# Performance work log

Hardware: AMD Instinct MI355X
Metric: run time of the kernel (lower is better)

## Reference

```python
import jax, jax.numpy as jnp
import numpy as np

B, T, D = 4, 2048, 1024
H, HS = 16, 64  # n_head, head_size


def setup_inputs() -> dict:
    key = jax.random.key(0)
    ks = jax.random.split(key, 6)
    s_in = 1.0 / np.sqrt(D)
    s_out = 1.0 / np.sqrt(H * HS)
    x = jax.random.normal(ks[0], (B, T, D), dtype=jnp.float32)
    Wq = jax.random.uniform(ks[1], (H, D, HS), jnp.float32, -s_in, s_in)
    Wk = jax.random.uniform(ks[2], (H, D, HS), jnp.float32, -s_in, s_in)
    Wv = jax.random.uniform(ks[3], (H, D, HS), jnp.float32, -s_in, s_in)
    Wo = jax.random.uniform(ks[4], (H * HS, D), jnp.float32, -s_out, s_out)
    bo = jax.random.uniform(ks[5], (D,), jnp.float32, -s_out, s_out)
    return {"x": x, "Wq": Wq, "Wk": Wk, "Wv": Wv, "Wo": Wo, "bo": bo}


def reference(x, Wq, Wk, Wv, Wo, bo):
    # per-head projections, batched across heads: [B,T,D] x [H,D,HS] -> [B,H,T,HS]
    q = jnp.einsum("btd,hde->bhte", x, Wq)
    k = jnp.einsum("btd,hde->bhte", x, Wk)
    v = jnp.einsum("btd,hde->bhte", x, Wv)
    scale = HS ** -0.5
    scores = jnp.einsum("bhqe,bhke->bhqk", q, k) * scale  # [B,H,T,T]
    causal = jnp.tril(jnp.ones((T, T), dtype=bool))
    scores = jnp.where(causal, scores, jnp.float32(-jnp.inf))
    attn = jax.nn.softmax(scores, axis=-1)
    out = jnp.einsum("bhqk,bhke->bhqe", attn, v)  # [B,H,T,HS]
    out = out.transpose(0, 2, 1, 3).reshape(B, T, H * HS)  # concat heads
    return out @ Wo + bo
```

## Files before the change

kernel.cpp:

```cpp
#include <hip/hip_runtime.h>

typedef __attribute__((ext_vector_type(8))) short short8v;
typedef __attribute__((ext_vector_type(4))) short short4v;
typedef __attribute__((ext_vector_type(4))) float floatx4;

namespace {
constexpr int Bn = 4, Tn = 2048, Dn = 1024, Hn = 16, HSn = 64;
}

__device__ __forceinline__ short f2bf(float f) {
  unsigned u = __builtin_bit_cast(unsigned, f);
  u += 0x7fffu + ((u >> 16) & 1u);
  return (short)(u >> 16);
}

__device__ __forceinline__ unsigned pkbf2(float lo, float hi) {
  unsigned r;
  asm("v_cvt_pk_bf16_f32 %0, %1, %2" : "=v"(r) : "v"(lo), "v"(hi));
  return r;
}

typedef const __attribute__((address_space(1))) unsigned int guint_t;
typedef __attribute__((address_space(3))) unsigned int luint_t;

__device__ __forceinline__ void gload16(const void* g, void* l) {
  __builtin_amdgcn_global_load_lds((guint_t*)g, (luint_t*)l, 16, 0, 0);
}

__device__ __forceinline__ short8v rd8(const char* base, int row, int kel) {
  return *(const short8v*)(base + row * 128 + ((kel * 2) ^ ((row & 7) << 4)));
}

__global__ __launch_bounds__(256) void cvt_x_k(const float* __restrict__ x, short* __restrict__ xb) {
  const size_t i = ((size_t)blockIdx.x * 256 + threadIdx.x) * 8;
  const float4 a = *(const float4*)(x + i);
  const float4 b = *(const float4*)(x + i + 4);
  short8v o;
  o[0] = f2bf(a.x); o[1] = f2bf(a.y); o[2] = f2bf(a.z); o[3] = f2bf(a.w);
  o[4] = f2bf(b.x); o[5] = f2bf(b.y); o[6] = f2bf(b.z); o[7] = f2bf(b.w);
  *(short8v*)(xb + i) = o;
}

__global__ __launch_bounds__(256) void tr_wqkv_k(const float* __restrict__ Wq, const float* __restrict__ Wk,
                                                 const float* __restrict__ Wv, short* __restrict__ wt) {
  const int ph = blockIdx.x;
  const int p = ph >> 4, h = ph & 15;
  const int dt = blockIdx.y;
  const float* W = p == 0 ? Wq : p == 1 ? Wk : Wv;
  __shared__ float T[64][65];
  const int t = threadIdx.x;
  const int rr = t >> 2, c0 = (t & 3) * 4;
  const float* src = W + (size_t)h * (Dn * HSn) + (size_t)(dt * 64 + rr) * HSn;
  #pragma unroll
  for (int q = 0; q < 4; ++q) {
    const float4 v = *(const float4*)(src + c0 + q * 16);
    T[rr][c0 + q * 16 + 0] = v.x; T[rr][c0 + q * 16 + 1] = v.y;
    T[rr][c0 + q * 16 + 2] = v.z; T[rr][c0 + q * 16 + 3] = v.w;
  }
  __syncthreads();
  short* dst = wt + ((size_t)p * 1024 + h * 64 + rr) * 1024 + dt * 64;
  #pragma unroll
  for (int q = 0; q < 4; ++q) {
    const int dl = c0 + q * 16;
    short4v ov = {f2bf(T[dl + 0][rr]), f2bf(T[dl + 1][rr]),
                  f2bf(T[dl + 2][rr]), f2bf(T[dl + 3][rr])};
    *(short4v*)(dst + dl) = ov;
  }
}

__global__ __launch_bounds__(256) void tr_wo_k(const float* __restrict__ Wo, short* __restrict__ wot) {
  const int ktile = blockIdx.x, ntile = blockIdx.y;
  __shared__ float T[64][65];
  const int t = threadIdx.x;
  const int rr = t >> 2, c0 = (t & 3) * 4;
  const float* src = Wo + (size_t)(ktile * 64 + rr) * Dn + ntile * 64;
  #pragma unroll
  for (int q = 0; q < 4; ++q) {
    const float4 v = *(const float4*)(src + c0 + q * 16);
    T[rr][c0 + q * 16 + 0] = v.x; T[rr][c0 + q * 16 + 1] = v.y;
    T[rr][c0 + q * 16 + 2] = v.z; T[rr][c0 + q * 16 + 3] = v.w;
  }
  __syncthreads();
  short* dst = wot + (size_t)(ntile * 64 + rr) * 1024 + ktile * 64;
  #pragma unroll
  for (int q = 0; q < 4; ++q) {
    const int dl = c0 + q * 16;
    short4v ov = {f2bf(T[dl + 0][rr]), f2bf(T[dl + 1][rr]),
                  f2bf(T[dl + 2][rr]), f2bf(T[dl + 3][rr])};
    *(short4v*)(dst + dl) = ov;
  }
}

__device__ __forceinline__ void gemm_mainloop(const char* gA, const char* gB, char* As, char* Bs,
                                              floatx4 acc[4][4]) {
  const int tid = threadIdx.x;
  const int wv = tid >> 6, ln = tid & 63;
  const int wr = wv >> 1, wc = wv & 1;
  const int lr = ln >> 3, lg = ln & 7;
  const int fr = ln & 15, kq = ln >> 4;
  for (int kt = 0; kt < 16; ++kt) {
    __syncthreads();
    #pragma unroll
    for (int c = 0; c < 4; ++c) {
      const int r = wv * 32 + c * 8 + lr;
      const int sw = (lg * 16) ^ ((r & 7) * 16);
      gload16(gA + (size_t)r * 2048 + kt * 128 + sw, As + (wv * 32 + c * 8) * 128);
      gload16(gB + (size_t)r * 2048 + kt * 128 + sw, Bs + (wv * 32 + c * 8) * 128);
    }
    __syncthreads();
    #pragma unroll
    for (int kb = 0; kb < 2; ++kb) {
      const int k0 = kb * 32 + kq * 8;
      short8v af[4], bfr[4];
      #pragma unroll
      for (int i = 0; i < 4; ++i) af[i] = rd8(As, wr * 64 + i * 16 + fr, k0);
      #pragma unroll
      for (int j = 0; j < 4; ++j) bfr[j] = rd8(Bs, wc * 64 + j * 16 + fr, k0);
      #pragma unroll
      for (int i = 0; i < 4; ++i)
        #pragma unroll
        for (int j = 0; j < 4; ++j)
          acc[i][j] = __builtin_amdgcn_mfma_f32_16x16x32_bf16(af[i], bfr[j], acc[i][j], 0, 0, 0);
    }
  }
}

__global__ __launch_bounds__(256) void gemm_qkv_k(const short* __restrict__ xb, const short* __restrict__ wt,
                                                  short* __restrict__ qb, short* __restrict__ kb,
                                                  short* __restrict__ vb) {
  __shared__ __align__(16) char As[16384];
  __shared__ __align__(16) char Bs[16384];
  const int m0 = blockIdx.x * 128, n0 = blockIdx.y * 128;
  floatx4 acc[4][4];
  #pragma unroll
  for (int i = 0; i < 4; ++i)
    #pragma unroll
    for (int j = 0; j < 4; ++j) acc[i][j] = floatx4{0.f, 0.f, 0.f, 0.f};
  gemm_mainloop((const char*)xb + (size_t)m0 * 2048, (const char*)wt + (size_t)n0 * 2048, As, Bs, acc);

  const int tid = threadIdx.x, wv = tid >> 6, ln = tid & 63;
  const int wr = wv >> 1, wc = wv & 1;
  const int proj = n0 >> 10;
  const int b = m0 >> 11;
  const int rb_ = (ln >> 4) * 4, fc = ln & 15;
  if (proj < 2) {
    short* dst = proj == 0 ? qb : kb;
    const float sc = proj == 0 ? 0.18033688011112042f : 1.0f;
    #pragma unroll
    for (int i = 0; i < 4; ++i) {
      const int m = m0 + wr * 64 + i * 16 + rb_;
      #pragma unroll
      for (int j = 0; j < 4; ++j) {
        const int n = n0 + wc * 64 + j * 16 + fc;
        const int h = (n >> 6) & 15, e = n & 63;
        short* dp = dst + ((size_t)(b * 16 + h) * Tn + (m & 2047)) * 64 + e;
        #pragma unroll
        for (int r = 0; r < 4; ++r) dp[(size_t)r * 64] = f2bf(acc[i][j][r] * sc);
      }
    }
  } else {
    #pragma unroll
    for (int i = 0; i < 4; ++i) {
      const int m = m0 + wr * 64 + i * 16 + rb_;
      const int t0 = m & 2047;
      #pragma unroll
      for (int j = 0; j < 4; ++j) {
        const int n = n0 + wc * 64 + j * 16 + fc;
        const int h = (n >> 6) & 15, e = n & 63;
        short4v ov = {f2bf(acc[i][j][0]), f2bf(acc[i][j][1]),
                      f2bf(acc[i][j][2]), f2bf(acc[i][j][3])};
        *(short4v*)(vb + ((size_t)(b * 16 + h) * 64 + e) * Tn + t0) = ov;
      }
    }
  }
}

__global__ __launch_bounds__(256) void attn_k(const short* __restrict__ qg, const short* __restrict__ kg,
                                              const short* __restrict__ vg, short* __restrict__ og) {
  __shared__ __align__(16) char Qs[16384];
  __shared__ __align__(16) char Ks[16384];
  __shared__ __align__(16) char Vs[16384];
  char* Ps = Qs;
  const int qt = gridDim.y - 1 - blockIdx.y;
  const int bh = blockIdx.x;
  const int tid = threadIdx.x, wv = tid >> 6, ln = tid & 63;
  const int lr = ln >> 3, lg = ln & 7;
  const int fr = ln & 15, kq = ln >> 4;
  const char* qbase = (const char*)qg + (size_t)bh * Tn * 128;
  const char* kbase = (const char*)kg + (size_t)bh * Tn * 128;
  const char* vbase = (const char*)vg + (size_t)bh * Tn * 128;

  #pragma unroll
  for (int c = 0; c < 4; ++c) {
    const int r = c * 32 + wv * 8 + lr;
    const int sw = (lg * 16) ^ ((r & 7) * 16);
    gload16(qbase + (size_t)(qt * 128 + r) * 128 + sw, Qs + (c * 32 + wv * 8) * 128);
  }
  #pragma unroll
  for (int c = 0; c < 2; ++c) {
    const int r = c * 32 + wv * 8 + lr;
    const int sw = (lg * 16) ^ ((r & 7) * 16);
    gload16(kbase + (size_t)r * 128 + sw, Ks + (c * 32 + wv * 8) * 128);
    gload16(vbase + (size_t)r * 4096 + sw, Vs + (c * 32 + wv * 8) * 128);
  }
  __syncthreads();

  short8v qf[2][2];
  #pragma unroll
  for (int c = 0; c < 2; ++c)
    #pragma unroll
    for (int kb = 0; kb < 2; ++kb)
      qf[c][kb] = rd8(Qs, wv * 32 + c * 16 + fr, kb * 32 + kq * 8);

  short8v ones8;
  #pragma unroll
  for (int i = 0; i < 8; ++i) ones8[i] = (short)0x3F80;

  floatx4 ot[4][2];
  #pragma unroll
  for (int f = 0; f < 4; ++f) { ot[f][0] = floatx4{0.f,0.f,0.f,0.f}; ot[f][1] = floatx4{0.f,0.f,0.f,0.f}; }
  floatx4 lacc[2] = {floatx4{0.f,0.f,0.f,0.f}, floatx4{0.f,0.f,0.f,0.f}};
  float m_i[2] = {-1e30f, -1e30f};

  const int nkt = 2 * qt + 2;
  const int q0w = qt * 128 + wv * 32;
  for (int kt = 0; kt < nkt; ++kt) {
    const int cur = kt & 1;
    if (kt + 1 < nkt) {
      #pragma unroll
      for (int c = 0; c < 2; ++c) {
        const int r = c * 32 + wv * 8 + lr;
        const int sw = (lg * 16) ^ ((r & 7) * 16);
        gload16(kbase + (size_t)((kt + 1) * 64 + r) * 128 + sw,
                Ks + (cur ^ 1) * 8192 + (c * 32 + wv * 8) * 128);
        gload16(vbase + (size_t)r * 4096 + (size_t)(kt + 1) * 128 + sw,
                Vs + (cur ^ 1) * 8192 + (c * 32 + wv * 8) * 128);
      }
    }
    if (kt * 64 <= q0w + 31) {
      const char* Ksc = Ks + cur * 8192;
      const char* Vsc = Vs + cur * 8192;
      floatx4 st[2][4];
      #pragma unroll
      for (int f = 0; f < 4; ++f) { st[0][f] = floatx4{0.f,0.f,0.f,0.f}; st[1][f] = floatx4{0.f,0.f,0.f,0.f}; }
      #pragma unroll
      for (int kb = 0; kb < 2; ++kb) {
        const int e0 = kb * 32 + kq * 8;
        #pragma unroll
        for (int f = 0; f < 4; ++f) {
          const short8v kf = rd8(Ksc, f * 16 + fr, e0);
          st[0][f] = __builtin_amdgcn_mfma_f32_16x16x32_bf16(kf, qf[0][kb], st[0][f], 0, 0, 0);
          st[1][f] = __builtin_amdgcn_mfma_f32_16x16x32_bf16(kf, qf[1][kb], st[1][f], 0, 0, 0);
        }
      }
      if (kt * 64 + 63 > q0w) {
        #pragma unroll
        for (int c = 0; c < 2; ++c) {
          const int q = q0w + c * 16 + fr;
          #pragma unroll
          for (int f = 0; f < 4; ++f)
            #pragma unroll
            for (int r = 0; r < 4; ++r)
              if (kt * 64 + f * 16 + kq * 4 + r > q) st[c][f][r] = -3.0e38f;
        }
      }
      float mx[2];
      #pragma unroll
      for (int c = 0; c < 2; ++c) {
        float v = fmaxf(fmaxf(st[c][0][0], st[c][0][1]), st[c][0][2]);
        v = fmaxf(fmaxf(v, st[c][0][3]), st[c][1][0]);
        v = fmaxf(fmaxf(v, st[c][1][1]), st[c][1][2]);
        v = fmaxf(fmaxf(v, st[c][1][3]), st[c][2][0]);
        v = fmaxf(fmaxf(v, st[c][2][1]), st[c][2][2]);
        v = fmaxf(fmaxf(v, st[c][2][3]), st[c][3][0]);
        v = fmaxf(fmaxf(v, st[c][3][1]), st[c][3][2]);
        v = fmaxf(v, st[c][3][3]);
        v = fmaxf(v, __shfl_xor(v, 16, 64));
        v = fmaxf(v, __shfl_xor(v, 32, 64));
        mx[c] = v;
      }
      const bool noresc = __all((mx[0] <= m_i[0] + 8.f) && (mx[1] <= m_i[1] + 8.f));
      if (!noresc) {
        #pragma unroll
        for (int c = 0; c < 2; ++c) {
          const float mn = fmaxf(m_i[c], mx[c]);
          const float al = exp2f(m_i[c] - mn);
          m_i[c] = mn;
          lacc[c] *= al;
          #pragma unroll
          for (int f = 0; f < 4; ++f) ot[f][c] *= al;
        }
      }
      #pragma unroll
      for (int c = 0; c < 2; ++c) {
        const int prow = wv * 32 + c * 16 + fr;
        #pragma unroll
        for (int f = 0; f < 4; ++f) {
          const float p0 = exp2f(st[c][f][0] - m_i[c]);
          const float p1 = exp2f(st[c][f][1] - m_i[c]);
          const float p2 = exp2f(st[c][f][2] - m_i[c]);
          const float p3 = exp2f(st[c][f][3] - m_i[c]);
          uint2 pv = {pkbf2(p0, p1), pkbf2(p2, p3)};
          *(uint2*)(Ps + prow * 128 + ((f * 32 + kq * 8) ^ ((prow & 7) * 16))) = pv;
        }
      }
      #pragma unroll
      for (int kb = 0; kb < 2; ++kb) {
        const int v0 = kb * 32 + kq * 8;
        const short8v pb0 = rd8(Ps, wv * 32 + fr, v0);
        const short8v pb1 = rd8(Ps, wv * 32 + 16 + fr, v0);
        lacc[0] = __builtin_amdgcn_mfma_f32_16x16x32_bf16(ones8, pb0, lacc[0], 0, 0, 0);
        lacc[1] = __builtin_amdgcn_mfma_f32_16x16x32_bf16(ones8, pb1, lacc[1], 0, 0, 0);
        #pragma unroll
        for (int f = 0; f < 4; ++f) {
          const short8v vf = rd8(Vsc, f * 16 + fr, v0);
          ot[f][0] = __builtin_amdgcn_mfma_f32_16x16x32_bf16(vf, pb0, ot[f][0], 0, 0, 0);
          ot[f][1] = __builtin_amdgcn_mfma_f32_16x16x32_bf16(vf, pb1, ot[f][1], 0, 0, 0);
        }
      }
    }
    __syncthreads();
  }

  const int b = bh >> 4, h = bh & 15;
  #pragma unroll
  for (int c = 0; c < 2; ++c) {
    const float inv = 1.0f / lacc[c][0];
    const size_t t = (size_t)(b * Tn + qt * 128 + wv * 32 + c * 16 + fr);
    #pragma unroll
    for (int f = 0; f < 4; ++f) {
      uint2 o4 = {pkbf2(ot[f][c][0] * inv, ot[f][c][1] * inv),
                  pkbf2(ot[f][c][2] * inv, ot[f][c][3] * inv)};
      *(uint2*)(og + t * 1024 + h * 64 + f * 16 + kq * 4) = o4;
    }
  }
}

__global__ __launch_bounds__(256) void gemm_out_k(const short* __restrict__ ao, const short* __restrict__ wot,
                                                  const float* __restrict__ bo, float* __restrict__ out) {
  __shared__ __align__(16) char As[16384];
  __shared__ __align__(16) char Bs[16384];
  const int m0 = blockIdx.x * 128, n0 = blockIdx.y * 128;
  floatx4 acc[4][4];
  #pragma unroll
  for (int i = 0; i < 4; ++i)
    #pragma unroll
    for (int j = 0; j < 4; ++j) acc[i][j] = floatx4{0.f, 0.f, 0.f, 0.f};
  gemm_mainloop((const char*)ao + (size_t)m0 * 2048, (const char*)wot + (size_t)n0 * 2048, As, Bs, acc);

  const int tid = threadIdx.x, wv = tid >> 6, ln = tid & 63;
  const int wr = wv >> 1, wc = wv & 1;
  const int rb_ = (ln >> 4) * 4, fc = ln & 15;
  #pragma unroll
  for (int i = 0; i < 4; ++i) {
    const int m = m0 + wr * 64 + i * 16 + rb_;
    #pragma unroll
    for (int j = 0; j < 4; ++j) {
      const int n = n0 + wc * 64 + j * 16 + fc;
      const float bias = bo[n];
      #pragma unroll
      for (int r = 0; r < 4; ++r) out[(size_t)(m + r) * Dn + n] = acc[i][j][r] + bias;
    }
  }
}

extern "C" void kernel_launch(void* const* d_in, const int* in_sizes, int n_in,
                              void* d_out, int out_size, void* d_ws, size_t ws_size,
                              hipStream_t stream) {
  const float* x  = (const float*)d_in[0];
  const float* Wq = (const float*)d_in[1];
  const float* Wk = (const float*)d_in[2];
  const float* Wv = (const float*)d_in[3];
  const float* Wo = (const float*)d_in[4];
  const float* bo = (const float*)d_in[5];
  float* out = (float*)d_out;

  char* ws = (char*)d_ws;
  short* xb  = (short*)(ws);
  short* wt  = (short*)(ws + (16u << 20));
  short* wot = (short*)(ws + (22u << 20));
  short* qb  = (short*)(ws + (24u << 20));
  short* kb  = (short*)(ws + (40u << 20));
  short* vb  = (short*)(ws + (56u << 20));
  short* ao  = (short*)(ws + (72u << 20));

  cvt_x_k<<<4096, 256, 0, stream>>>(x, xb);
  tr_wqkv_k<<<dim3(48, 16), 256, 0, stream>>>(Wq, Wk, Wv, wt);
  tr_wo_k<<<dim3(16, 16), 256, 0, stream>>>(Wo, wot);
  gemm_qkv_k<<<dim3(64, 24), 256, 0, stream>>>(xb, wt, qb, kb, vb);
  attn_k<<<dim3(64, 16), 256, 0, stream>>>(qb, kb, vb, ao);
  gemm_out_k<<<dim3(64, 8), 256, 0, stream>>>(ao, wot, bo, out);
}
```

Measured before the change: 190.2 us.

## Keep softmax probabilities in registers and drop Q/P shared-memory staging

The exp'd probability tile is no longer written to and re-read from LDS. The MFMA B operand is built directly from the S accumulator registers, with the key-index order permuted to match the accumulator layout. V fragments are gathered as two 8-byte LDS reads so the permutation holds on that side too. Q is loaded straight from global into registers, removing the Q LDS buffer, and launch bounds request 4 blocks per SM. This saves LDS traffic and a shared round trip, and the smaller LDS footprint raises occupancy, at the cost of narrower V reads and possible register pressure.

```diff
diff --git a/kernel.cpp b/kernel.cpp
--- a/kernel.cpp
+++ b/kernel.cpp
@@ -3,6 +3,8 @@
 typedef __attribute__((ext_vector_type(8))) short short8v;
 typedef __attribute__((ext_vector_type(4))) short short4v;
 typedef __attribute__((ext_vector_type(4))) float floatx4;
+typedef __attribute__((ext_vector_type(4))) unsigned uint4v;
+typedef __attribute__((ext_vector_type(2))) unsigned long long ulong2v;
 
 namespace {
 constexpr int Bn = 4, Tn = 2048, Dn = 1024, Hn = 16, HSn = 64;
@@ -175,12 +177,10 @@
   }
 }
 
-__global__ __launch_bounds__(256) void attn_k(const short* __restrict__ qg, const short* __restrict__ kg,
-                                              const short* __restrict__ vg, short* __restrict__ og) {
-  __shared__ __align__(16) char Qs[16384];
+__global__ __launch_bounds__(256, 4) void attn_k(const short* __restrict__ qg, const short* __restrict__ kg,
+                                                 const short* __restrict__ vg, short* __restrict__ og) {
   __shared__ __align__(16) char Ks[16384];
   __shared__ __align__(16) char Vs[16384];
-  char* Ps = Qs;
   const int qt = gridDim.y - 1 - blockIdx.y;
   const int bh = blockIdx.x;
   const int tid = threadIdx.x, wv = tid >> 6, ln = tid & 63;
@@ -191,26 +191,20 @@
   const char* vbase = (const char*)vg + (size_t)bh * Tn * 128;
 
   #pragma unroll
-  for (int c = 0; c < 4; ++c) {
-    const int r = c * 32 + wv * 8 + lr;
-    const int sw = (lg * 16) ^ ((r & 7) * 16);
-    gload16(qbase + (size_t)(qt * 128 + r) * 128 + sw, Qs + (c * 32 + wv * 8) * 128);
-  }
-  #pragma unroll
   for (int c = 0; c < 2; ++c) {
     const int r = c * 32 + wv * 8 + lr;
     const int sw = (lg * 16) ^ ((r & 7) * 16);
     gload16(kbase + (size_t)r * 128 + sw, Ks + (c * 32 + wv * 8) * 128);
     gload16(vbase + (size_t)r * 4096 + sw, Vs + (c * 32 + wv * 8) * 128);
   }
-  __syncthreads();
-
+
+  const char* qrow0 = qbase + (size_t)(qt * 128 + wv * 32) * 128;
   short8v qf[2][2];
   #pragma unroll
   for (int c = 0; c < 2; ++c)
     #pragma unroll
     for (int kb = 0; kb < 2; ++kb)
-      qf[c][kb] = rd8(Qs, wv * 32 + c * 16 + fr, kb * 32 + kq * 8);
+      qf[c][kb] = *(const short8v*)(qrow0 + (c * 16 + fr) * 128 + kb * 64 + kq * 16);
 
   short8v ones8;
   #pragma unroll
@@ -222,8 +216,11 @@
   floatx4 lacc[2] = {floatx4{0.f,0.f,0.f,0.f}, floatx4{0.f,0.f,0.f,0.f}};
   float m_i[2] = {-1e30f, -1e30f};
 
+  const int swz = (fr & 7) * 16;
   const int nkt = 2 * qt + 2;
   const int q0w = qt * 128 + wv * 32;
+  __syncthreads();
+
   for (int kt = 0; kt < nkt; ++kt) {
     const int cur = kt & 1;
     if (kt + 1 < nkt) {
@@ -291,31 +288,36 @@
           for (int f = 0; f < 4; ++f) ot[f][c] *= al;
         }
       }
-      #pragma unroll
-      for (int c = 0; c < 2; ++c) {
-        const int prow = wv * 32 + c * 16 + fr;
+      short8v pbv[2][2];
+      #pragma unroll
+      for (int c = 0; c < 2; ++c)
+        #pragma unroll
+        for (int kb = 0; kb < 2; ++kb) {
+          uint4v u;
+          u[0] = pkbf2(exp2f(st[c][kb][0] - m_i[c]),     exp2f(st[c][kb][1] - m_i[c]));
+          u[1] = pkbf2(exp2f(st[c][kb][2] - m_i[c]),     exp2f(st[c][kb][3] - m_i[c]));
+          u[2] = pkbf2(exp2f(st[c][kb + 2][0] - m_i[c]), exp2f(st[c][kb + 2][1] - m_i[c]));
+          u[3] = pkbf2(exp2f(st[c][kb + 2][2] - m_i[c]), exp2f(st[c][kb + 2][3] - m_i[c]));
+          pbv[c][kb] = __builtin_bit_cast(short8v, u);
+        }
+      #pragma unroll
+      for (int kb = 0; kb < 2; ++kb) {
+        lacc[0] = __builtin_amdgcn_mfma_f32_16x16x32_bf16(ones8, pbv[0][kb], lacc[0], 0, 0, 0);
+        lacc[1] = __builtin_amdgcn_mfma_f32_16x16x32_bf16(ones8, pbv[1][kb], lacc[1], 0, 0, 0);
+      }
+      #pragma unroll
+      for (int kb = 0; kb < 2; ++kb) {
+        const int blo = (kb * 32 + kq * 8) ^ swz;
+        const int bhi = (kb * 32 + 64 + kq * 8) ^ swz;
         #pragma unroll
         for (int f = 0; f < 4; ++f) {
-          const float p0 = exp2f(st[c][f][0] - m_i[c]);
-          const float p1 = exp2f(st[c][f][1] - m_i[c]);
-          const float p2 = exp2f(st[c][f][2] - m_i[c]);
-          const float p3 = exp2f(st[c][f][3] - m_i[c]);
-          uint2 pv = {pkbf2(p0, p1), pkbf2(p2, p3)};
-          *(uint2*)(Ps + prow * 128 + ((f * 32 + kq * 8) ^ ((prow & 7) * 16))) = pv;
-        }
-      }
-      #pragma unroll
-      for (int kb = 0; kb < 2; ++kb) {
-        const int v0 = kb * 32 + kq * 8;
-        const short8v pb0 = rd8(Ps, wv * 32 + fr, v0);
-        const short8v pb1 = rd8(Ps, wv * 32 + 16 + fr, v0);
-        lacc[0] = __builtin_amdgcn_mfma_f32_16x16x32_bf16(ones8, pb0, lacc[0], 0, 0, 0);
-        lacc[1] = __builtin_amdgcn_mfma_f32_16x16x32_bf16(ones8, pb1, lacc[1], 0, 0, 0);
-        #pragma unroll
-        for (int f = 0; f < 4; ++f) {
-          const short8v vf = rd8(Vsc, f * 16 + fr, v0);
-          ot[f][0] = __builtin_amdgcn_mfma_f32_16x16x32_bf16(vf, pb0, ot[f][0], 0, 0, 0);
-          ot[f][1] = __builtin_amdgcn_mfma_f32_16x16x32_bf16(vf, pb1, ot[f][1], 0, 0, 0);
+          const char* vrow = Vsc + (f * 16 + fr) * 128;
+          ulong2v vv;
+          vv[0] = *(const unsigned long long*)(vrow + blo);
+          vv[1] = *(const unsigned long long*)(vrow + bhi);
+          const short8v vf = __builtin_bit_cast(short8v, vv);
+          ot[f][0] = __builtin_amdgcn_mfma_f32_16x16x32_bf16(vf, pbv[0][kb], ot[f][0], 0, 0, 0);
+          ot[f][1] = __builtin_amdgcn_mfma_f32_16x16x32_bf16(vf, pbv[1][kb], ot[f][1], 0, 0, 0);
         }
       }
     }
```

New measurement: 173.0 us. 9.1% less time.
